# Optimization experiments

Measured on AMD Instinct MI355X. Metric: run time of the kernel, lower is better.

Reference implementation:

```python
import jax, jax.numpy as jnp
import numpy as np

ALPHA = 0.2  # leaky relu slope
NEG = -1e9


def setup_inputs() -> dict:
    key = jax.random.key(0)
    ks = jax.random.split(key, 8)
    B, N, F_IN, H, HID, OUT = 2, 4096, 512, 4, 128, 64
    x = jax.random.normal(ks[0], (B, N, F_IN), dtype=jnp.float32)
    adj = jax.random.randint(ks[1], (B, N, N), 0, 2, dtype=jnp.int32)
    s_in = float(np.sqrt(2.0 / (F_IN + HID)))
    W_heads = jax.random.normal(ks[2], (H, HID, F_IN), dtype=jnp.float32) * s_in
    a1_heads = jax.random.normal(ks[3], (H, HID), dtype=jnp.float32) * 0.1
    a2_heads = jax.random.normal(ks[4], (H, HID), dtype=jnp.float32) * 0.1
    s_out = float(np.sqrt(2.0 / (H * HID + OUT)))
    W_out = jax.random.normal(ks[5], (OUT, H * HID), dtype=jnp.float32) * s_out
    a1_out = jax.random.normal(ks[6], (OUT,), dtype=jnp.float32) * 0.1
    a2_out = jax.random.normal(ks[7], (OUT,), dtype=jnp.float32) * 0.1
    return {"x": x, "adj": adj, "W_heads": W_heads, "a1_heads": a1_heads,
            "a2_heads": a2_heads, "W_out": W_out, "a1_out": a1_out, "a2_out": a2_out}


def _gat_layer(x, adj, W, a1, a2, concat):
    # x: [B,N,F], W: [O,F], a1/a2: [O]
    h = jnp.einsum('bnf,of->bno', x, W)            # [B,N,O]
    f1 = jnp.einsum('bno,o->bn', h, a1)            # [B,N]
    f2 = jnp.einsum('bno,o->bn', h, a2)            # [B,N]
    e = f1[:, :, None] + f2[:, None, :]            # [B,N,N] additive scores
    e = jnp.where(e > 0, e, ALPHA * e)             # leaky relu
    e = jnp.where(adj == 0, NEG, e)                # adjacency mask
    att = jax.nn.softmax(e, axis=2)
    h_prime = jnp.einsum('bnm,bmo->bno', att, h)
    return jax.nn.elu(h_prime) if concat else h_prime


def reference(x, adj, W_heads, a1_heads, a2_heads, W_out, a1_out, a2_out):
    H = W_heads.shape[0]
    heads = [_gat_layer(x, adj, W_heads[i], a1_heads[i], a2_heads[i], True)
             for i in range(H)]
    x_cat = jnp.concatenate(heads, axis=2)         # [B,N,H*HID]
    return _gat_layer(x_cat, adj, W_out, a1_out, a2_out, False)
```

## Files before the change

kernel.cpp:

```cpp
#include <hip/hip_runtime.h>

#define TB 2
#define TN 4096
#define TH 4
#define THID 128
#define TOUT 64
#define NW 128

using f4    = __attribute__((ext_vector_type(4))) float;
using s16x8 = __attribute__((ext_vector_type(8))) short;
using s16x4 = __attribute__((ext_vector_type(4))) short;
using u32x4 = __attribute__((ext_vector_type(4))) unsigned;

static __device__ __forceinline__ short f2bf(float f){
  unsigned u = __float_as_uint(f);
  unsigned r = u + 0x7FFFu + ((u >> 16) & 1u);
  return (short)(r >> 16);
}
static __device__ __forceinline__ float bf2f(short s){
  return __uint_as_float(((unsigned)(unsigned short)s) << 16);
}
static __device__ __forceinline__ unsigned encf(float f){
  unsigned u = __float_as_uint(f);
  return (u & 0x80000000u) ? ~u : (u | 0x80000000u);
}
static __device__ __forceinline__ float decf(unsigned u){
  unsigned v = (u & 0x80000000u) ? (u & 0x7FFFFFFFu) : ~u;
  return __uint_as_float(v);
}
static __device__ __forceinline__ void gll16(const void* g, void* l){
  __builtin_amdgcn_global_load_lds((const __attribute__((address_space(1))) unsigned int*)g,
                                   (__attribute__((address_space(3))) unsigned int*)l, 16, 0, 0);
}
static __device__ __forceinline__ f4 mfma_bf16(s16x8 a, s16x8 b, f4 c){
  return __builtin_amdgcn_mfma_f32_16x16x32_bf16(a, b, c, 0, 0, 0);
}

__global__ void k_prep(const int* __restrict__ adj, unsigned* __restrict__ adjp,
                       unsigned* __restrict__ mx,
                       const float* __restrict__ x, short* __restrict__ xh, short* __restrict__ xl,
                       const float* __restrict__ Wh, short* __restrict__ wh, short* __restrict__ wl,
                       const float* __restrict__ Wo, short* __restrict__ wo){
  int bid = blockIdx.x, tid = threadIdx.x;
  if (bid == 0 && tid < 16) mx[tid] = 0;
  if (bid < 4096){
    int t = bid * 256 + tid;
    f4 v = ((const f4*)x)[t];
    s16x4 h, l;
#pragma unroll
    for (int e = 0; e < 4; ++e){
      short hb = f2bf(v[e]);
      h[e] = hb;
      l[e] = f2bf(v[e] - bf2f(hb));
    }
    ((s16x4*)xh)[t] = h;
    ((s16x4*)xl)[t] = l;
  } else if (bid < 8192){
    int t = (bid - 4096) * 256 + tid;
    const int4* p = (const int4*)adj + (size_t)t * 8;
    unsigned m = 0;
#pragma unroll
    for (int i = 0; i < 8; ++i){
      int4 v = p[i];
      m |= (v.x != 0 ? 1u : 0u) << (i*4+0);
      m |= (v.y != 0 ? 1u : 0u) << (i*4+1);
      m |= (v.z != 0 ? 1u : 0u) << (i*4+2);
      m |= (v.w != 0 ? 1u : 0u) << (i*4+3);
    }
    adjp[t] = m;
  } else if (bid < 8448){
    int t = (bid - 8192) * 256 + tid;
    f4 v = ((const f4*)Wh)[t];
    s16x4 h, l;
#pragma unroll
    for (int e = 0; e < 4; ++e){
      short hb = f2bf(v[e]);
      h[e] = hb;
      l[e] = f2bf(v[e] - bf2f(hb));
    }
    ((s16x4*)wh)[t] = h;
    ((s16x4*)wl)[t] = l;
  } else {
    int t = (bid - 8448) * 256 + tid;
    f4 v = ((const f4*)Wo)[t];
    s16x4 h;
#pragma unroll
    for (int e = 0; e < 4; ++e) h[e] = f2bf(v[e]);
    ((s16x4*)wo)[t] = h;
  }
}

__global__ __launch_bounds__(512, 2) void k_gemm1(
    const short* __restrict__ xh, const short* __restrict__ xl,
    const short* __restrict__ wh, const short* __restrict__ wl,
    const float* __restrict__ a1h, const float* __restrict__ a2h,
    short* __restrict__ hTb, float* __restrict__ f1g,
    float* __restrict__ Qa, float* __restrict__ Sa, unsigned* __restrict__ mx){
  __shared__ short tiles[2][4][8192];
  __shared__ float red[2][128][2];
  __shared__ float bmx[2];
  int tid = threadIdx.x, lane = tid & 63, w = tid >> 6;
  int kgrp = lane >> 4, li = lane & 15;
  int nblk = blockIdx.x >> 6, mblk = blockIdx.x & 63;
  int n0 = nblk * 128, m0 = mblk * 128;
  int wn = w >> 2, wm = w & 3;
  const f4 fz = {0.f, 0.f, 0.f, 0.f};
  f4 acc[4][2];
#pragma unroll
  for (int i = 0; i < 4; ++i)
#pragma unroll
    for (int j = 0; j < 2; ++j) acc[i][j] = fz;

#pragma unroll
  for (int tno = 0; tno < 4; ++tno){
    const short* gb = (tno==0 ? wh : tno==1 ? wl : tno==2 ? xh : xl);
    int r0 = (tno < 2) ? n0 : m0;
#pragma unroll
    for (int i = 0; i < 2; ++i){
      int s = (i*8 + w)*64 + lane;
      int row = s >> 3, c = s & 7, cs = c ^ (row & 7);
      gll16(gb + (size_t)(r0 + row)*512 + cs*8, (char*)tiles[0][tno] + (i*8+w)*1024);
    }
  }
  asm volatile("s_waitcnt vmcnt(0)" ::: "memory");
  __syncthreads();

  for (int kt = 0; kt < 8; ++kt){
    int cur = kt & 1;
    if (kt < 7){
      int k0 = (kt+1) * 64;
#pragma unroll
      for (int tno = 0; tno < 4; ++tno){
        const short* gb = (tno==0 ? wh : tno==1 ? wl : tno==2 ? xh : xl);
        int r0 = (tno < 2) ? n0 : m0;
#pragma unroll
        for (int i = 0; i < 2; ++i){
          int s = (i*8 + w)*64 + lane;
          int row = s >> 3, c = s & 7, cs = c ^ (row & 7);
          gll16(gb + (size_t)(r0 + row)*512 + k0 + cs*8, (char*)tiles[cur^1][tno] + (i*8+w)*1024);
        }
      }
    }
    const char* t0 = (const char*)tiles[cur][0];
    const char* t1 = (const char*)tiles[cur][1];
    const char* t2 = (const char*)tiles[cur][2];
    const char* t3 = (const char*)tiles[cur][3];
#pragma unroll
    for (int ks = 0; ks < 2; ++ks){
      int ck = ks*4 + kgrp;
      s16x8 ah[4], al[4], bh[2], bl[2];
#pragma unroll
      for (int fn = 0; fn < 4; ++fn){
        int row = wn*64 + fn*16 + li;
        int off = row*128 + ((ck ^ (row & 7)) << 4);
        ah[fn] = *(const s16x8*)(t0 + off);
        al[fn] = *(const s16x8*)(t1 + off);
      }
#pragma unroll
      for (int fm = 0; fm < 2; ++fm){
        int row = wm*32 + fm*16 + li;
        int off = row*128 + ((ck ^ (row & 7)) << 4);
        bh[fm] = *(const s16x8*)(t2 + off);
        bl[fm] = *(const s16x8*)(t3 + off);
      }
#pragma unroll
      for (int fn = 0; fn < 4; ++fn)
#pragma unroll
        for (int fm = 0; fm < 2; ++fm)
          acc[fn][fm] = mfma_bf16(ah[fn], bh[fm], acc[fn][fm]);
#pragma unroll
      for (int fn = 0; fn < 4; ++fn)
#pragma unroll
        for (int fm = 0; fm < 2; ++fm)
          acc[fn][fm] = mfma_bf16(ah[fn], bl[fm], acc[fn][fm]);
#pragma unroll
      for (int fn = 0; fn < 4; ++fn)
#pragma unroll
        for (int fm = 0; fm < 2; ++fm)
          acc[fn][fm] = mfma_bf16(al[fn], bh[fm], acc[fn][fm]);
    }
    asm volatile("s_waitcnt vmcnt(0)" ::: "memory");
    __syncthreads();
  }
  int head = nblk;
#pragma unroll
  for (int fn = 0; fn < 4; ++fn){
#pragma unroll
    for (int fm = 0; fm < 2; ++fm){
#pragma unroll
      for (int r = 0; r < 4; ++r){
        int nout = n0 + wn*64 + fn*16 + kgrp*4 + r;
        int m = m0 + wm*32 + fm*16 + li;
        int b = m >> 12, n = m & 4095;
        int hid = nout & 127;
        size_t idx = ((size_t)((b*TH + head)*THID + hid))*TN + n;
        hTb[idx] = f2bf(acc[fn][fm][r]);
      }
    }
  }
  const float* a1p = a1h + head*THID;
  const float* a2p = a2h + head*THID;
  float s1[2] = {0.f, 0.f}, s2[2] = {0.f, 0.f};
#pragma unroll
  for (int fn = 0; fn < 4; ++fn)
#pragma unroll
    for (int r = 0; r < 4; ++r){
      int row = wn*64 + fn*16 + kgrp*4 + r;
      float w1 = a1p[row], w2 = a2p[row];
#pragma unroll
      for (int fm = 0; fm < 2; ++fm){
        s1[fm] = fmaf(acc[fn][fm][r], w1, s1[fm]);
        s2[fm] = fmaf(acc[fn][fm][r], w2, s2[fm]);
      }
    }
#pragma unroll
  for (int fm = 0; fm < 2; ++fm){
    s1[fm] += __shfl_xor(s1[fm], 16); s1[fm] += __shfl_xor(s1[fm], 32);
    s2[fm] += __shfl_xor(s2[fm], 16); s2[fm] += __shfl_xor(s2[fm], 32);
  }
  if (kgrp == 0){
#pragma unroll
    for (int fm = 0; fm < 2; ++fm){
      int col = wm*32 + fm*16 + li;
      red[wn][col][0] = s1[fm];
      red[wn][col][1] = s2[fm];
    }
  }
  __syncthreads();
  if (tid < 128){
    float f1v = red[0][tid][0] + red[1][tid][0];
    float f2v = red[0][tid][1] + red[1][tid][1];
    int m = m0 + tid, b = m >> 12, n = m & 4095;
    int idx = (b*TH + head)*TN + n;
    f1g[idx] = f1v;
    Qa[idx] = expf(f2v);
    Sa[idx] = expf(0.2f*f2v);
    float wmx = f2v;
#pragma unroll
    for (int d = 1; d < 64; d <<= 1) wmx = fmaxf(wmx, __shfl_xor(wmx, d));
    if ((tid & 63) == 0) bmx[tid >> 6] = wmx;
  }
  __syncthreads();
  if (tid == 0){
    int b = m0 >> 12;
    atomicMax(&mx[b*TH + head], encf(fmaxf(bmx[0], bmx[1])));
  }
}

__global__ __launch_bounds__(256, 2) void k_attn1(
    const short* __restrict__ hTb, const float* __restrict__ f1,
    const float* __restrict__ Qa, const float* __restrict__ Sa,
    const unsigned* __restrict__ adjp, const unsigned* __restrict__ mx,
    short* __restrict__ part, float* __restrict__ sums){
  __shared__ short tile[2][8192];
  __shared__ float Qs[1024], Ss[1024];
  int tid = threadIdx.x, lane = tid & 63, w = tid >> 6;
  int kgrp = lane >> 4, li = lane & 15;
  int bid = blockIdx.x;
  int js = bid >> 7, b = (bid >> 6) & 1, h = (bid >> 4) & 3, rblk = bid & 15;
  int bh = b*TH + h;
  int jbase = js * 1024;
  int r0b = rblk * 256;
  const short* hbase = hTb + ((size_t)bh*THID)*TN;
  const float* Qrow = Qa + (size_t)bh*TN + jbase;
  const float* Srow = Sa + (size_t)bh*TN + jbase;

  auto STAGE = [&](int t, char* dst){
    int jg = jbase + t*64;
#pragma unroll
    for (int i = 0; i < 4; ++i){
      int s = (i*4 + w)*64 + lane;
      int row = s >> 3, c = s & 7, cs = c ^ (row & 7);
      gll16(hbase + (size_t)row*TN + jg + cs*8, dst + (i*4+w)*1024);
    }
  };

  gll16(Qrow + w*256 + lane*4, (char*)Qs + w*1024);
  gll16(Srow + w*256 + lane*4, (char*)Ss + w*1024);
  STAGE(0, (char*)tile[0]);

  int r0 = r0b + w*64;
  float Pv[4], Rv[4];
  int rowa[4];
  float mf = decf(mx[bh]);
#pragma unroll
  for (int rf = 0; rf < 4; ++rf){
    int row = r0 + rf*16 + li;
    rowa[rf] = row;
    float f1v = f1[bh*TN + row];
    float e = f1v + mf;
    float m = e > 0.f ? e : 0.2f*e;
    Pv[rf] = expf(f1v - m);
    Rv[rf] = expf(0.2f*f1v - m);
  }
  const f4 fz = {0.f,0.f,0.f,0.f};
  f4 acc[4][8];
#pragma unroll
  for (int i = 0; i < 4; ++i)
#pragma unroll
    for (int j = 0; j < 8; ++j) acc[i][j] = fz;
  f4 accs[4] = {fz, fz, fz, fz};
  s16x8 ones;
#pragma unroll
  for (int e = 0; e < 8; ++e) ones[e] = (short)0x3F80;

  uint2 awc[4], awn[4];
#pragma unroll
  for (int rf = 0; rf < 4; ++rf)
    awc[rf] = *(const uint2*)&adjp[(size_t)(b*TN + rowa[rf])*NW + (jbase >> 5)];

  asm volatile("s_waitcnt vmcnt(0)" ::: "memory");
  __syncthreads();

  for (int jt = 0; jt < 16; ++jt){
    int cur = jt & 1;
    if (jt < 15){
      STAGE(jt+1, (char*)tile[cur^1]);
      int jg = jbase + (jt+1)*64;
#pragma unroll
      for (int rf = 0; rf < 4; ++rf)
        awn[rf] = *(const uint2*)&adjp[(size_t)(b*TN + rowa[rf])*NW + (jg >> 5)];
    }
    int j0 = jt*64;
    const char* tp = (const char*)tile[cur];
#pragma unroll
    for (int ks = 0; ks < 2; ++ks){
      int jloc = j0 + ks*32 + kgrp*8;
      float qv[8], sv[8];
      *(f4*)&qv[0] = *(const f4*)&Qs[jloc];
      *(f4*)&qv[4] = *(const f4*)&Qs[jloc+4];
      *(f4*)&sv[0] = *(const f4*)&Ss[jloc];
      *(f4*)&sv[4] = *(const f4*)&Ss[jloc+4];
      s16x8 af[4];
#pragma unroll
      for (int rf = 0; rf < 4; ++rf){
        unsigned word = ks ? awc[rf].y : awc[rf].x;
        unsigned byt = (word >> (kgrp*8)) & 0xFFu;
        float P = Pv[rf], R = Rv[rf];
        u32x4 pw;
#pragma unroll
        for (int pe = 0; pe < 4; ++pe){
          float va = fmaxf(P*qv[2*pe],   R*sv[2*pe]);
          float vb = fmaxf(P*qv[2*pe+1], R*sv[2*pe+1]);
          va = (byt & (1u << (2*pe)))   ? va : 0.f;
          vb = (byt & (1u << (2*pe+1))) ? vb : 0.f;
          unsigned ua = __float_as_uint(va) + 0x8000u;
          unsigned ub = __float_as_uint(vb) + 0x8000u;
          pw[pe] = __builtin_amdgcn_perm(ub, ua, 0x07060302);
        }
        af[rf] = __builtin_bit_cast(s16x8, pw);
      }
#pragma unroll
      for (int rf = 0; rf < 4; ++rf)
        accs[rf] = mfma_bf16(af[rf], ones, accs[rf]);
#pragma unroll
      for (int cf = 0; cf < 8; ++cf){
        int col = cf*16 + li;
        int off = col*128 + (((ks*4 + kgrp) ^ (col & 7)) << 4);
        s16x8 bfr = *(const s16x8*)(tp + off);
#pragma unroll
        for (int rf = 0; rf < 4; ++rf)
          acc[rf][cf] = mfma_bf16(af[rf], bfr, acc[rf][cf]);
      }
    }
    asm volatile("s_waitcnt vmcnt(0)" ::: "memory");
    __syncthreads();
#pragma unroll
    for (int rf = 0; rf < 4; ++rf) awc[rf] = awn[rf];
  }
  int sl = js*8 + bh;
  if (li == 0){
#pragma unroll
    for (int rf = 0; rf < 4; ++rf)
#pragma unroll
      for (int r = 0; r < 4; ++r)
        sums[(size_t)sl*TN + r0 + rf*16 + kgrp*4 + r] = accs[rf][r];
  }
#pragma unroll
  for (int rf = 0; rf < 4; ++rf)
#pragma unroll
    for (int cf = 0; cf < 8; ++cf)
#pragma unroll
      for (int r = 0; r < 4; ++r){
        int row = r0 + rf*16 + kgrp*4 + r;
        int hid = cf*16 + li;
        part[((size_t)sl*TN + row)*THID + hid] = f2bf(acc[rf][cf][r]);
      }
}

__global__ __launch_bounds__(128) void k_cg2(
    const short* __restrict__ part1, const float* __restrict__ sums1,
    const short* __restrict__ wo,
    const float* __restrict__ a1o, const float* __restrict__ a2o,
    short* __restrict__ h2T, float* __restrict__ f1o,
    float* __restrict__ Q2, float* __restrict__ S2, unsigned* __restrict__ mx2){
  __shared__ short xs[32*512];
  int tid = threadIdx.x, lane = tid & 63, w = tid >> 6;
  int kgrp = lane >> 4, li = lane & 15;
  int m0 = blockIdx.x * 32;
  for (int it = 0; it < 16; ++it){
    int idx = it*128 + tid;
    int r = idx >> 6, c8 = idx & 63;
    int row = m0 + r, b = row >> 12, n = row & 4095;
    int h = c8 >> 4, hid8 = c8 & 15;
    float a[8] = {0,0,0,0,0,0,0,0};
    float s = 0.f;
#pragma unroll
    for (int js = 0; js < 4; ++js){
      size_t rowoff = (size_t)(js*8 + b*TH + h)*TN + n;
      s16x8 pv = *(const s16x8*)(part1 + rowoff*THID + hid8*8);
#pragma unroll
      for (int e = 0; e < 8; ++e) a[e] += bf2f(pv[e]);
      s += sums1[rowoff];
    }
    float inv = 1.f / s;
    s16x8 o;
#pragma unroll
    for (int e = 0; e < 8; ++e){
      float xv = a[e] * inv;
      o[e] = f2bf(xv > 0.f ? xv : expm1f(xv));
    }
    *(s16x8*)((char*)xs + r*1024 + ((c8*16) ^ ((r & 7) << 4))) = o;
  }
  __syncthreads();
  const f4 fz = {0.f,0.f,0.f,0.f};
  f4 acc[4] = {fz, fz, fz, fz};
  int rowL = w*16 + li;
  for (int kt = 0; kt < 16; ++kt){
    int k = kt*32 + kgrp*8;
    s16x8 a = *(const s16x8*)((const char*)xs + rowL*1024 + ((k*2) ^ ((rowL & 7) << 4)));
#pragma unroll
    for (int cf = 0; cf < 4; ++cf){
      int col = cf*16 + li;
      s16x8 bfr = *(const s16x8*)(wo + (size_t)col*512 + k);
      acc[cf] = mfma_bf16(a, bfr, acc[cf]);
    }
  }
  float p1[4] = {0,0,0,0}, p2[4] = {0,0,0,0};
#pragma unroll
  for (int cf = 0; cf < 4; ++cf){
    int o = cf*16 + li;
    float w1 = a1o[o], w2 = a2o[o];
#pragma unroll
    for (int r = 0; r < 4; ++r){
      p1[r] = fmaf(acc[cf][r], w1, p1[r]);
      p2[r] = fmaf(acc[cf][r], w2, p2[r]);
    }
  }
#pragma unroll
  for (int r = 0; r < 4; ++r){
#pragma unroll
    for (int d = 1; d < 16; d <<= 1){
      p1[r] += __shfl_xor(p1[r], d);
      p2[r] += __shfl_xor(p2[r], d);
    }
  }
#pragma unroll
  for (int cf = 0; cf < 4; ++cf)
#pragma unroll
    for (int r = 0; r < 4; ++r){
      int row = m0 + w*16 + kgrp*4 + r;
      int o = cf*16 + li;
      int b = row >> 12, n = row & 4095;
      h2T[((size_t)(b*TOUT + o))*TN + n] = f2bf(acc[cf][r]);
    }
  if (li == 0){
#pragma unroll
    for (int r = 0; r < 4; ++r){
      int row = m0 + w*16 + kgrp*4 + r;
      f1o[row] = p1[r];
      Q2[row] = expf(p2[r]);
      S2[row] = expf(0.2f*p2[r]);
    }
  }
  float m2 = fmaxf(fmaxf(p2[0], p2[1]), fmaxf(p2[2], p2[3]));
  m2 = fmaxf(m2, __shfl_xor(m2, 16));
  m2 = fmaxf(m2, __shfl_xor(m2, 32));
  __shared__ float bm[2];
  if (lane == 0) bm[w] = m2;
  __syncthreads();
  if (tid == 0) atomicMax(&mx2[m0 >> 12], encf(fmaxf(bm[0], bm[1])));
}

__global__ __launch_bounds__(256, 2) void k_attn2(
    const short* __restrict__ h2T, const float* __restrict__ f1o,
    const float* __restrict__ Q2, const float* __restrict__ S2,
    const unsigned* __restrict__ adjp, const unsigned* __restrict__ mx2,
    float* __restrict__ part, float* __restrict__ sums){
  __shared__ short tile[2][4096];
  __shared__ float Qs[512], Ss[512];
  int tid = threadIdx.x, lane = tid & 63, w = tid >> 6;
  int kgrp = lane >> 4, li = lane & 15;
  int bid = blockIdx.x;
  int js = bid >> 6, b = (bid >> 5) & 1, rblk = bid & 31;
  int jbase = js * 512;
  int r0b = rblk * 128;
  const short* hbase = h2T + (size_t)b*TOUT*TN;
  const float* Qrow = Q2 + (size_t)b*TN + jbase;
  const float* Srow = S2 + (size_t)b*TN + jbase;

  auto STAGE = [&](int t, char* dst){
    int jg = jbase + t*64;
#pragma unroll
    for (int i = 0; i < 2; ++i){
      int s = (i*4 + w)*64 + lane;
      int row = s >> 3, c = s & 7, cs = c ^ (row & 7);
      gll16(hbase + (size_t)row*TN + jg + cs*8, dst + (i*4+w)*1024);
    }
  };

  if (w < 2) gll16(Qrow + w*256 + lane*4, (char*)Qs + w*1024);
  else       gll16(Srow + (w-2)*256 + lane*4, (char*)Ss + (w-2)*1024);
  STAGE(0, (char*)tile[0]);

  int r0 = r0b + w*32;
  float Pv[2], Rv[2];
  int rowa[2];
  float mf = decf(mx2[b]);
#pragma unroll
  for (int rf = 0; rf < 2; ++rf){
    int row = r0 + rf*16 + li;
    rowa[rf] = row;
    float f1v = f1o[b*TN + row];
    float e = f1v + mf;
    float m = e > 0.f ? e : 0.2f*e;
    Pv[rf] = expf(f1v - m);
    Rv[rf] = expf(0.2f*f1v - m);
  }
  const f4 fz = {0.f,0.f,0.f,0.f};
  f4 acc[2][4];
#pragma unroll
  for (int i = 0; i < 2; ++i)
#pragma unroll
    for (int j = 0; j < 4; ++j) acc[i][j] = fz;
  f4 accs[2] = {fz, fz};
  s16x8 ones;
#pragma unroll
  for (int e = 0; e < 8; ++e) ones[e] = (short)0x3F80;

  uint2 awc[2], awn[2];
#pragma unroll
  for (int rf = 0; rf < 2; ++rf)
    awc[rf] = *(const uint2*)&adjp[(size_t)(b*TN + rowa[rf])*NW + (jbase >> 5)];

  asm volatile("s_waitcnt vmcnt(0)" ::: "memory");
  __syncthreads();

  for (int jt = 0; jt < 8; ++jt){
    int cur = jt & 1;
    if (jt < 7){
      STAGE(jt+1, (char*)tile[cur^1]);
      int jg = jbase + (jt+1)*64;
#pragma unroll
      for (int rf = 0; rf < 2; ++rf)
        awn[rf] = *(const uint2*)&adjp[(size_t)(b*TN + rowa[rf])*NW + (jg >> 5)];
    }
    int j0 = jt*64;
    const char* tp = (const char*)tile[cur];
#pragma unroll
    for (int ks = 0; ks < 2; ++ks){
      int jloc = j0 + ks*32 + kgrp*8;
      float qv[8], sv[8];
      *(f4*)&qv[0] = *(const f4*)&Qs[jloc];
      *(f4*)&qv[4] = *(const f4*)&Qs[jloc+4];
      *(f4*)&sv[0] = *(const f4*)&Ss[jloc];
      *(f4*)&sv[4] = *(const f4*)&Ss[jloc+4];
      s16x8 af[2];
#pragma unroll
      for (int rf = 0; rf < 2; ++rf){
        unsigned word = ks ? awc[rf].y : awc[rf].x;
        unsigned byt = (word >> (kgrp*8)) & 0xFFu;
        float P = Pv[rf], R = Rv[rf];
        u32x4 pw;
#pragma unroll
        for (int pe = 0; pe < 4; ++pe){
          float va = fmaxf(P*qv[2*pe],   R*sv[2*pe]);
          float vb = fmaxf(P*qv[2*pe+1], R*sv[2*pe+1]);
          va = (byt & (1u << (2*pe)))   ? va : 0.f;
          vb = (byt & (1u << (2*pe+1))) ? vb : 0.f;
          unsigned ua = __float_as_uint(va) + 0x8000u;
          unsigned ub = __float_as_uint(vb) + 0x8000u;
          pw[pe] = __builtin_amdgcn_perm(ub, ua, 0x07060302);
        }
        af[rf] = __builtin_bit_cast(s16x8, pw);
      }
      accs[0] = mfma_bf16(af[0], ones, accs[0]);
      accs[1] = mfma_bf16(af[1], ones, accs[1]);
#pragma unroll
      for (int cf = 0; cf < 4; ++cf){
        int col = cf*16 + li;
        int off = col*128 + (((ks*4 + kgrp) ^ (col & 7)) << 4);
        s16x8 bfr = *(const s16x8*)(tp + off);
        acc[0][cf] = mfma_bf16(af[0], bfr, acc[0][cf]);
        acc[1][cf] = mfma_bf16(af[1], bfr, acc[1][cf]);
      }
    }
    asm volatile("s_waitcnt vmcnt(0)" ::: "memory");
    __syncthreads();
    awc[0] = awn[0]; awc[1] = awn[1];
  }
  int sl = js*2 + b;
  if (li == 0){
#pragma unroll
    for (int rf = 0; rf < 2; ++rf)
#pragma unroll
      for (int r = 0; r < 4; ++r)
        sums[(size_t)sl*TN + r0 + rf*16 + kgrp*4 + r] = accs[rf][r];
  }
#pragma unroll
  for (int rf = 0; rf < 2; ++rf)
#pragma unroll
    for (int cf = 0; cf < 4; ++cf)
#pragma unroll
      for (int r = 0; r < 4; ++r){
        int row = r0 + rf*16 + kgrp*4 + r;
        int o = cf*16 + li;
        part[((size_t)sl*TN + row)*TOUT + o] = acc[rf][cf][r];
      }
}

__global__ void k_comb2(const float* __restrict__ part, const float* __restrict__ sums,
                        float* __restrict__ out){
  int t = blockIdx.x*256 + threadIdx.x;
  int o4 = t & 15, n = (t >> 4) & 4095, b = t >> 16;
  f4 a = {0.f,0.f,0.f,0.f};
  float s = 0.f;
#pragma unroll
  for (int js = 0; js < 8; ++js){
    int sl = js*2 + b;
    a += ((const f4*)part)[((size_t)sl*TN + n)*16 + o4];
    s += sums[(size_t)sl*TN + n];
  }
  f4 r = a / s;
  ((f4*)out)[((size_t)(b*TN + n))*16 + o4] = r;
}

extern "C" void kernel_launch(void* const* d_in, const int* in_sizes, int n_in,
                              void* d_out, int out_size, void* d_ws, size_t ws_size,
                              hipStream_t stream) {
  (void)in_sizes; (void)n_in; (void)out_size; (void)ws_size;
  const float* x       = (const float*)d_in[0];
  const int*   adj     = (const int*)d_in[1];
  const float* W_heads = (const float*)d_in[2];
  const float* a1h     = (const float*)d_in[3];
  const float* a2h     = (const float*)d_in[4];
  const float* W_out   = (const float*)d_in[5];
  const float* a1o     = (const float*)d_in[6];
  const float* a2o     = (const float*)d_in[7];

  char* p = (char*)d_ws;
  auto alloc = [&](size_t sz){ char* r = p; p += (sz + 255) & ~(size_t)255; return r; };
  unsigned* adjp  = (unsigned*) alloc(4ull*1048576);
  short*    wo    = (short*)    alloc(2ull*32768);
  short*    hTb   = (short*)    alloc(2ull*4194304);
  float*    f1    = (float*)    alloc(4ull*32768);
  float*    Qa    = (float*)    alloc(4ull*32768);
  float*    Sa    = (float*)    alloc(4ull*32768);
  unsigned* mx    = (unsigned*) alloc(4ull*16);
  float*    f1o   = (float*)    alloc(4ull*8192);
  float*    Q2    = (float*)    alloc(4ull*8192);
  float*    S2    = (float*)    alloc(4ull*8192);
  short*    h2T   = (short*)    alloc(2ull*524288);
  float*    sums1 = (float*)    alloc(4ull*131072);
  float*    sums2 = (float*)    alloc(4ull*65536);
  char* A = alloc(33554432ull);
  short* xh   = (short*)A;
  short* xl   = (short*)(A + 8388608);
  short* part1 = (short*)A;
  char* Bu = alloc(16777216ull);
  short* wh = (short*)Bu;
  short* wl = (short*)(Bu + 524288);
  float* part2 = (float*)Bu;

  k_prep <<<8480, 256, 0, stream>>>(adj, adjp, mx, x, xh, xl, W_heads, wh, wl, W_out, wo);
  k_gemm1<<<256, 512, 0, stream>>>(xh, xl, wh, wl, a1h, a2h, hTb, f1, Qa, Sa, mx);
  k_attn1<<<512, 256, 0, stream>>>(hTb, f1, Qa, Sa, adjp, mx, part1, sums1);
  k_cg2  <<<256, 128, 0, stream>>>(part1, sums1, wo, a1o, a2o, h2T, f1o, Q2, S2, mx + 8);
  k_attn2<<<512, 256, 0, stream>>>(h2T, f1o, Q2, S2, adjp, mx + 8, part2, sums2);
  k_comb2<<<512, 256, 0, stream>>>(part2, sums2, (float*)d_out);
}
```

Baseline: 152.7 us.

## Move adjacency bit-packing into GEMM1 launch as extra blocks, coalesce loads

The adjacency packing is taken out of the prep kernel and run as extra blocks appended to the first GEMM launch. Those blocks read the int adjacency with lane-contiguous, coalesced int4 loads and build each 32-bit mask with wave shuffles. The aim is to overlap the bandwidth-bound 128 MiB adjacency read with the compute-bound GEMM and to improve load coalescing. The GEMM's launch bounds drop from 2 to 1 blocks per CU, which could change register allocation and occupancy for the GEMM blocks.

```diff
diff --git a/kernel.cpp b/kernel.cpp
--- a/kernel.cpp
+++ b/kernel.cpp
@@ -36,8 +36,7 @@
   return __builtin_amdgcn_mfma_f32_16x16x32_bf16(a, b, c, 0, 0, 0);
 }
 
-__global__ void k_prep(const int* __restrict__ adj, unsigned* __restrict__ adjp,
-                       unsigned* __restrict__ mx,
+__global__ void k_prep(unsigned* __restrict__ mx,
                        const float* __restrict__ x, short* __restrict__ xh, short* __restrict__ xl,
                        const float* __restrict__ Wh, short* __restrict__ wh, short* __restrict__ wl,
                        const float* __restrict__ Wo, short* __restrict__ wo){
@@ -55,21 +54,8 @@
     }
     ((s16x4*)xh)[t] = h;
     ((s16x4*)xl)[t] = l;
-  } else if (bid < 8192){
+  } else if (bid < 4352){
     int t = (bid - 4096) * 256 + tid;
-    const int4* p = (const int4*)adj + (size_t)t * 8;
-    unsigned m = 0;
-#pragma unroll
-    for (int i = 0; i < 8; ++i){
-      int4 v = p[i];
-      m |= (v.x != 0 ? 1u : 0u) << (i*4+0);
-      m |= (v.y != 0 ? 1u : 0u) << (i*4+1);
-      m |= (v.z != 0 ? 1u : 0u) << (i*4+2);
-      m |= (v.w != 0 ? 1u : 0u) << (i*4+3);
-    }
-    adjp[t] = m;
-  } else if (bid < 8448){
-    int t = (bid - 8192) * 256 + tid;
     f4 v = ((const f4*)Wh)[t];
     s16x4 h, l;
 #pragma unroll
@@ -81,7 +67,7 @@
     ((s16x4*)wh)[t] = h;
     ((s16x4*)wl)[t] = l;
   } else {
-    int t = (bid - 8448) * 256 + tid;
+    int t = (bid - 4352) * 256 + tid;
     f4 v = ((const f4*)Wo)[t];
     s16x4 h;
 #pragma unroll
@@ -90,12 +76,42 @@
   }
 }
 
-__global__ __launch_bounds__(512, 2) void k_gemm1(
+__global__ __launch_bounds__(512, 1) void k_gemm1(
     const short* __restrict__ xh, const short* __restrict__ xl,
     const short* __restrict__ wh, const short* __restrict__ wl,
     const float* __restrict__ a1h, const float* __restrict__ a2h,
+    const int* __restrict__ adj, unsigned* __restrict__ adjp,
     short* __restrict__ hTb, float* __restrict__ f1g,
     float* __restrict__ Qa, float* __restrict__ Sa, unsigned* __restrict__ mx){
+  if (blockIdx.x >= 256){
+    int pb = blockIdx.x - 256;
+    int lane = threadIdx.x & 63, w = threadIdx.x >> 6;
+    int gw0 = pb*512 + w*64;
+    const int4* base = (const int4*)adj + (size_t)gw0*8;
+    int4 v[8];
+#pragma unroll
+    for (int i = 0; i < 8; ++i) v[i] = base[i*64 + lane];
+    unsigned nib[8];
+#pragma unroll
+    for (int i = 0; i < 8; ++i){
+      unsigned nb = (v[i].x != 0 ? 1u : 0u) | (v[i].y != 0 ? 2u : 0u)
+                  | (v[i].z != 0 ? 4u : 0u) | (v[i].w != 0 ? 8u : 0u);
+      nib[i] = nb << (4*(lane & 7));
+    }
+#pragma unroll
+    for (int i = 0; i < 8; ++i){
+      nib[i] |= __shfl_xor(nib[i], 1);
+      nib[i] |= __shfl_xor(nib[i], 2);
+      nib[i] |= __shfl_xor(nib[i], 4);
+    }
+    if ((lane & 7) == 0){
+      int sub = lane >> 3;
+#pragma unroll
+      for (int i = 0; i < 8; ++i)
+        adjp[gw0 + i*8 + sub] = nib[i];
+    }
+    return;
+  }
   __shared__ short tiles[2][4][8192];
   __shared__ float red[2][128][2];
   __shared__ float bmx[2];
@@ -672,8 +688,8 @@
   short* wl = (short*)(Bu + 524288);
   float* part2 = (float*)Bu;
 
-  k_prep <<<8480, 256, 0, stream>>>(adj, adjp, mx, x, xh, xl, W_heads, wh, wl, W_out, wo);
-  k_gemm1<<<256, 512, 0, stream>>>(xh, xl, wh, wl, a1h, a2h, hTb, f1, Qa, Sa, mx);
+  k_prep <<<4384, 256, 0, stream>>>(mx, x, xh, xl, W_heads, wh, wl, W_out, wo);
+  k_gemm1<<<2304, 512, 0, stream>>>(xh, xl, wh, wl, a1h, a2h, adj, adjp, hTb, f1, Qa, Sa, mx);
   k_attn1<<<512, 256, 0, stream>>>(hTb, f1, Qa, Sa, adjp, mx, part1, sums1);
   k_cg2  <<<256, 128, 0, stream>>>(part1, sums1, wo, a1o, a2o, h2T, f1o, Q2, S2, mx + 8);
   k_attn2<<<512, 256, 0, stream>>>(h2T, f1o, Q2, S2, adjp, mx + 8, part2, sums2);
```

Result: no change. 151.7 us (-0.6%).
